# Optimization experiments

Hardware: AMD Instinct MI355X
Metric: run time of the kernel (lower is better)

## Reference

```python
import jax, jax.numpy as jnp
import numpy as np

B, Q, WAY, SHOT, H, W, C = 2, 75, 5, 5, 10, 10, 640
NEIGHBOR_K = 5


def setup_inputs() -> dict:
    key = jax.random.key(0)
    k1, k2 = jax.random.split(key)
    input1 = jax.random.normal(k1, (B, Q, H, W, C), dtype=jnp.float32)
    # per the original unpacking: dim1=shot, dim2=way
    input2 = jax.random.normal(k2, (B, SHOT, WAY, H, W, C), dtype=jnp.float32)
    return {"input1": input1, "input2": input2, "neighbor_k": NEIGHBOR_K}


def reference(input1, input2, neighbor_k):
    # input1: [b, q_num, h, w, c] query local descriptors
    # input2: [b, shot, way, h, w, c] support local descriptors
    b, q_num, h, w, c = input1.shape
    _, shot, way, _, _, _ = input2.shape
    hw = h * w

    q = input1.reshape(b, q_num, hw, c)
    s = input2.reshape(b, way * shot, hw, c)

    # L2-normalize each local descriptor over channel dim
    q = q / jnp.linalg.norm(q, axis=-1, keepdims=True)
    s = s / jnp.linalg.norm(s, axis=-1, keepdims=True)

    # group support descriptors per class: [b, way, shot*hw, c]
    # (matches torch .view semantics on the contiguous flattened buffer)
    support = s.reshape(b, way, shot * hw, c)

    # cosine similarity between every query patch and every support patch
    # scores: [b, q_num, way, hw, shot*hw]
    scores = jnp.einsum('bqpc,bwsc->bqwps', q, support)

    # top-k nearest support descriptors per query patch, mean over k
    topv, _ = jax.lax.top_k(scores, neighbor_k)          # [b,q,way,hw,k]
    sim_local = jnp.sum(topv, axis=-1) / neighbor_k      # [b,q,way,hw]
    sim_way = jnp.sum(sim_local, axis=-1)                # [b,q,way]
    return sim_way
```

## Files before the change

### kernel.cpp

```cpp
#include <hip/hip_runtime.h>

#define QN    75
#define HWN   100
#define CN    640
#define NSUP  500
#define MROWS 7500
#define NQD   (2 * MROWS)
#define NSD   5000
#define NDESC (NQD + NSD)
#define MT    128
#define NT    256
#define BK    32
#define HBUF  24576
#define CST   272

typedef __attribute__((ext_vector_type(8))) __bf16 bf16x8;
typedef __attribute__((ext_vector_type(4))) float  f32x4;

#define GLDS(gp, lp) __builtin_amdgcn_global_load_lds(                        \
    (const __attribute__((address_space(1))) void*)(gp),                      \
    (__attribute__((address_space(3))) void*)(lp), 16, 0, 0)

static __device__ inline unsigned short f2bf(float f) {
    unsigned int u = __float_as_uint(f);
    u += 0x7fffu + ((u >> 16) & 1u);
    return (unsigned short)(u >> 16);
}

__global__ __launch_bounds__(256) void prep_kernel(const float* __restrict__ q,
                                                   const float* __restrict__ s,
                                                   unsigned short* __restrict__ qbf,
                                                   unsigned short* __restrict__ sbf) {
    int wave = (blockIdx.x * 256 + threadIdx.x) >> 6;
    int lane = threadIdx.x & 63;
    if (wave >= NDESC) return;
    const float* src = (wave < NQD) ? (q + (size_t)wave * CN)
                                    : (s + (size_t)(wave - NQD) * CN);
    unsigned short* dst = (wave < NQD) ? (qbf + (size_t)wave * CN)
                                       : (sbf + (size_t)(wave - NQD) * CN);
    float4 v[3];
    float ss = 0.f;
#pragma unroll
    for (int j = 0; j < 3; ++j) {
        int idx4 = lane + 64 * j;
        if (idx4 < CN / 4) {
            v[j] = *(const float4*)(src + idx4 * 4);
            ss = fmaf(v[j].x, v[j].x, ss);
            ss = fmaf(v[j].y, v[j].y, ss);
            ss = fmaf(v[j].z, v[j].z, ss);
            ss = fmaf(v[j].w, v[j].w, ss);
        }
    }
#pragma unroll
    for (int off = 32; off > 0; off >>= 1)
        ss += __shfl_xor(ss, off, 64);
    float inv = rsqrtf(ss);
#pragma unroll
    for (int j = 0; j < 3; ++j) {
        int idx4 = lane + 64 * j;
        if (idx4 < CN / 4) {
            ushort4 o;
            o.x = f2bf(v[j].x * inv);
            o.y = f2bf(v[j].y * inv);
            o.z = f2bf(v[j].z * inv);
            o.w = f2bf(v[j].w * inv);
            *(ushort4*)(dst + idx4 * 4) = o;
        }
    }
}

__global__ __launch_bounds__(512, 4) void mfma_kernel(const unsigned short* __restrict__ qbf,
                                                      const unsigned short* __restrict__ sbf,
                                                      float* __restrict__ part) {
    const int xcd = blockIdx.x & 7;
    const int idx = blockIdx.x >> 3;
    const int b   = xcd >> 2;
    const int mbq = xcd & 3;
    const int mbsz = (mbq < 3) ? 15 : 14;
    if (idx >= 10 * mbsz) return;
    const int g  = idx / (2 * mbsz);
    const int r_ = idx % (2 * mbsz);
    const int nc = r_ / mbsz;
    const int mb = mbq * 15 + (r_ % mbsz);
    const int bg = b * 5 + g;
    const int r0 = mb * MT;
    const int c0 = nc * NT;

    __shared__ __align__(16) char smem[2 * HBUF];
    float* Cst = (float*)smem;

    const int t    = threadIdx.x;
    const int lane = t & 63;
    const int wid  = t >> 6;
    const int h    = wid >> 2;
    const int colq = wid & 3;

    const unsigned short* qptr = qbf + (size_t)b * MROWS * CN;
    const unsigned short* sptr = sbf + (size_t)(b * 25 + g * 5) * HWN * CN;

    f32x4 acc[4][4];
#pragma unroll
    for (int mt = 0; mt < 4; ++mt)
#pragma unroll
        for (int nt = 0; nt < 4; ++nt)
            acc[mt][nt] = (f32x4)0.f;

    const int lxr  = lane >> 2;
    const int lg   = lane & 3;
    const int gsrc = lg ^ ((lxr ^ (lxr >> 2)) & 3);

    int ar = r0 + wid * 16 + lxr;            if (ar > MROWS - 1) ar = MROWS - 1;
    const int aoff = ar * CN + gsrc * 8;
    int bc0 = c0 + wid * 32 + lxr;           if (bc0 > NSUP - 1) bc0 = NSUP - 1;
    int bc1 = c0 + wid * 32 + 16 + lxr;      if (bc1 > NSUP - 1) bc1 = NSUP - 1;
    const int boff0 = bc0 * CN + gsrc * 8;
    const int boff1 = bc1 * CN + gsrc * 8;

    const int q_ = lane >> 4;
    const int lr = lane & 15;
    const int sl = (q_ ^ ((lr ^ (lr >> 2)) & 3)) * 8;

#define STAGE(base, kk)                                                        \
    {                                                                          \
        char* ad = smem + (base) + wid * 1024;                                 \
        char* bd = smem + (base) + 8192 + wid * 2048;                          \
        GLDS(qptr + aoff  + (kk), ad);                                         \
        GLDS(sptr + boff0 + (kk), bd);                                         \
        GLDS(sptr + boff1 + (kk), bd + 1024);                                  \
    }

#define COMPUTE(base)                                                          \
    {                                                                          \
        const unsigned short* Al = (const unsigned short*)(smem + (base));     \
        const unsigned short* Bl = Al + 4096;                                  \
        bf16x8 af[4];                                                          \
        _Pragma("unroll")                                                      \
        for (int mt = 0; mt < 4; ++mt)                                         \
            af[mt] = *(const bf16x8*)(Al + (h * 64 + mt * 16 + lr) * 32 + sl); \
        _Pragma("unroll")                                                      \
        for (int nt = 0; nt < 4; ++nt) {                                       \
            bf16x8 bfr = *(const bf16x8*)(Bl + (colq * 64 + nt * 16 + lr) * 32 + sl); \
            _Pragma("unroll")                                                  \
            for (int mt = 0; mt < 4; ++mt)                                     \
                acc[mt][nt] = __builtin_amdgcn_mfma_f32_16x16x32_bf16(af[mt], bfr, acc[mt][nt], 0, 0, 0); \
        }                                                                      \
    }

    STAGE(0, 0);
    __syncthreads();
#pragma unroll 3
    for (int k2 = 0; k2 < 9; ++k2) {
        const int kk = k2 * 2;
        STAGE(HBUF, (kk + 1) * BK);
        COMPUTE(0);
        __syncthreads();
        STAGE(0, (kk + 2) * BK);
        COMPUTE(HBUF);
        __syncthreads();
    }
    STAGE(HBUF, 19 * BK);
    COMPUTE(0);
    __syncthreads();
    COMPUTE(HBUF);
#undef STAGE
#undef COMPUTE

    const int erow = t >> 4;
    const int es   = t & 15;
#define CE(a, b) { float hi_ = fmaxf(a, b), lo_ = fminf(a, b); a = hi_; b = lo_; }
#pragma unroll
    for (int mt = 0; mt < 4; ++mt) {
        __syncthreads();
#pragma unroll
        for (int nt = 0; nt < 4; ++nt)
#pragma unroll
            for (int e = 0; e < 4; ++e)
                Cst[(h * 16 + q_ * 4 + e) * CST + colq * 64 + nt * 16 + lr] = acc[mt][nt][e];
        __syncthreads();

        float t0 = -3.4e38f, t1 = -3.4e38f, t2 = -3.4e38f, t3 = -3.4e38f, t4 = -3.4e38f;
#pragma unroll
        for (int i = 0; i < 16; ++i) {
            int col = es + 16 * i;
            float v = (c0 + col < NSUP) ? Cst[erow * CST + col] : -3.4e38f;
            float hi;
            hi = fmaxf(t0, v); v = fminf(t0, v); t0 = hi;
            hi = fmaxf(t1, v); v = fminf(t1, v); t1 = hi;
            hi = fmaxf(t2, v); v = fminf(t2, v); t2 = hi;
            hi = fmaxf(t3, v); v = fminf(t3, v); t3 = hi;
            hi = fmaxf(t4, v); v = fminf(t4, v); t4 = hi;
        }
#pragma unroll
        for (int d = 1; d < 16; d <<= 1) {
            float b0 = __shfl_xor(t0, d, 64);
            float b1 = __shfl_xor(t1, d, 64);
            float b2 = __shfl_xor(t2, d, 64);
            float b3 = __shfl_xor(t3, d, 64);
            float b4 = __shfl_xor(t4, d, 64);
            t0 = fmaxf(t0, b4); t1 = fmaxf(t1, b3); t2 = fmaxf(t2, b2);
            t3 = fmaxf(t3, b1); t4 = fmaxf(t4, b0);
            CE(t0, t1); CE(t2, t3);
            CE(t1, t2); CE(t3, t4);
            CE(t0, t1); CE(t2, t3);
            CE(t1, t2); CE(t3, t4);
            CE(t0, t1); CE(t2, t3);
        }
        if (es == 0) {
            int patch = r0 + (erow >> 4) * 64 + mt * 16 + (erow & 15);
            if (patch < MROWS) {
                float* pp = part + ((size_t)(bg * MROWS + patch) * 2 + nc) * 5;
                pp[0] = t0; pp[1] = t1; pp[2] = t2; pp[3] = t3; pp[4] = t4;
            }
        }
    }
#undef CE
}

__global__ __launch_bounds__(256) void merge_kernel(const float* __restrict__ part,
                                                    float* __restrict__ out) {
    int w    = (blockIdx.x * 256 + threadIdx.x) >> 6;
    int lane = threadIdx.x & 63;
    if (w >= 750) return;
    int b  = w / 375, r = w % 375;
    int qi = r / 5,   g = r % 5;
    int bg = b * 5 + g;

    float sum = 0.f;
    for (int p = lane; p < HWN; p += 64) {
        int row = qi * HWN + p;
        const float* pp = part + (size_t)(bg * MROWS + row) * 10;
        float t0 = -3.4e38f, t1 = -3.4e38f, t2 = -3.4e38f, t3 = -3.4e38f, t4 = -3.4e38f;
#pragma unroll
        for (int j = 0; j < 10; ++j) {
            float v = pp[j], hi;
            hi = fmaxf(t0, v); v = fminf(t0, v); t0 = hi;
            hi = fmaxf(t1, v); v = fminf(t1, v); t1 = hi;
            hi = fmaxf(t2, v); v = fminf(t2, v); t2 = hi;
            hi = fmaxf(t3, v); v = fminf(t3, v); t3 = hi;
            hi = fmaxf(t4, v); v = fminf(t4, v); t4 = hi;
        }
        sum += (t0 + t1 + t2 + t3 + t4) * 0.2f;
    }
#pragma unroll
    for (int off = 32; off > 0; off >>= 1)
        sum += __shfl_xor(sum, off, 64);
    if (lane == 0) out[w] = sum;
}

extern "C" void kernel_launch(void* const* d_in, const int* in_sizes, int n_in,
                              void* d_out, int out_size, void* d_ws, size_t ws_size,
                              hipStream_t stream) {
    const float* in1 = (const float*)d_in[0];
    const float* in2 = (const float*)d_in[1];
    float* out = (float*)d_out;

    unsigned short* qbf  = (unsigned short*)d_ws;
    unsigned short* sbf  = qbf + (size_t)NQD * CN;
    float*          part = (float*)(sbf + (size_t)NSD * CN);

    prep_kernel<<<dim3(NDESC / 4), 256, 0, stream>>>(in1, in2, qbf, sbf);
    mfma_kernel<<<dim3(1200), 512, 0, stream>>>(qbf, sbf, part);
    merge_kernel<<<dim3(188), 256, 0, stream>>>(part, out);
}
```

Baseline: 163.8 us.

## Switch K-loop to triple-buffered LDS pipeline with single barrier per step

Replaces the double-buffered K loop with a three-buffer rotation that issues global-to-LDS loads two steps ahead. It waits with a partial vmcnt so only the oldest stage must land before each barrier, and uses one barrier per step instead of two. This targets load latency and barrier stalls in the GEMM main loop. LDS use grows by half, which may reduce resident blocks per CU.

```diff
diff --git a/kernel.cpp b/kernel.cpp
--- a/kernel.cpp
+++ b/kernel.cpp
@@ -86,7 +86,7 @@
     const int r0 = mb * MT;
     const int c0 = nc * NT;
 
-    __shared__ __align__(16) char smem[2 * HBUF];
+    __shared__ __align__(16) char smem[3 * HBUF];
     float* Cst = (float*)smem;
 
     const int t    = threadIdx.x;
@@ -146,22 +146,32 @@
         }                                                                      \
     }
 
+#define ITER(tt, CB, SB)                                                       \
+    {                                                                          \
+        asm volatile("s_waitcnt vmcnt(3)" ::: "memory");   \
+        __builtin_amdgcn_sched_barrier(0);                                     \
+        __builtin_amdgcn_s_barrier();         \
+        STAGE((SB) * HBUF, (tt + 2) * BK);               \
+        COMPUTE((CB) * HBUF);                 \
+    }
+
     STAGE(0, 0);
-    __syncthreads();
-#pragma unroll 3
-    for (int k2 = 0; k2 < 9; ++k2) {
-        const int kk = k2 * 2;
-        STAGE(HBUF, (kk + 1) * BK);
-        COMPUTE(0);
-        __syncthreads();
-        STAGE(0, (kk + 2) * BK);
-        COMPUTE(HBUF);
-        __syncthreads();
-    }
-    STAGE(HBUF, 19 * BK);
+    STAGE(HBUF, BK);
+#pragma unroll 1
+    for (int tb = 0; tb < 18; tb += 3) {
+        ITER(tb + 0, 0, 2);
+        ITER(tb + 1, 1, 0);
+        ITER(tb + 2, 2, 1);
+    }
+    asm volatile("s_waitcnt vmcnt(3)" ::: "memory");
+    __builtin_amdgcn_sched_barrier(0);
+    __builtin_amdgcn_s_barrier();
     COMPUTE(0);
-    __syncthreads();
+    asm volatile("s_waitcnt vmcnt(0)" ::: "memory");
+    __builtin_amdgcn_sched_barrier(0);
+    __builtin_amdgcn_s_barrier();
     COMPUTE(HBUF);
+#undef ITER
 #undef STAGE
 #undef COMPUTE
 
```

After: 164.1 us. About the same (+0.2%).
